# Optimization experiments

Hardware: AMD Instinct MI355X
Metric: run time of the kernel (lower is better)

Reference implementation:

```python
import jax, jax.numpy as jnp
import numpy as np

B, T, C = 2, 2048, 1024
H = 16
D = C // H          # 64
HID = C // 4        # meta_net bottleneck = 256
FF = 4 * C          # 4096


def setup_inputs() -> dict:
    key = jax.random.key(0)
    ks = jax.random.split(key, 11)
    s = lambda fan_in: 1.0 / np.sqrt(fan_in)
    inp = {
        "x": jax.random.normal(ks[0], (B, T, C), jnp.float32),
        # torch nn.Linear weights are [out, in]
        "Wq": jax.random.uniform(ks[1], (C, C), jnp.float32, -s(C), s(C)),
        "Wk": jax.random.uniform(ks[2], (C, C), jnp.float32, -s(C), s(C)),
        "Wv": jax.random.uniform(ks[3], (C, C), jnp.float32, -s(C), s(C)),
        "Wm1": jax.random.uniform(ks[4], (HID, C), jnp.float32, -s(C), s(C)),
        "bm1": jax.random.uniform(ks[5], (HID,), jnp.float32, -s(C), s(C)),
        "Wm2": jax.random.uniform(ks[6], (H, HID), jnp.float32, -s(HID), s(HID)),
        "bm2": jax.random.uniform(ks[7], (H,), jnp.float32, -s(HID), s(HID)),
        "Wproj": jax.random.uniform(ks[8], (C, C), jnp.float32, -s(C), s(C)),
        "Wfc": jax.random.uniform(ks[9], (FF, C), jnp.float32, -s(C), s(C)),
        "Wcp": jax.random.uniform(ks[10], (C, FF), jnp.float32, -s(FF), s(FF)),
    }
    return inp


def _rms_norm(x):
    eps = jnp.finfo(x.dtype).eps
    return x * jax.lax.rsqrt(jnp.mean(jnp.square(x), axis=-1, keepdims=True) + eps)


def reference(x, Wq, Wk, Wv, Wm1, bm1, Wm2, bm2, Wproj, Wfc, Wcp):
    b, t, c = x.shape
    h = Wm2.shape[0]
    d = c // h
    q = (x @ Wq.T).reshape(b, t, h, d)
    k = (x @ Wk.T).reshape(b, t, h, d)
    v = (x @ Wv.T).reshape(b, t, h, d)
    surprise = jax.nn.sigmoid(jnp.maximum(x @ Wm1.T + bm1, 0.0) @ Wm2.T + bm2)  # [b,t,h]
    decay = 1.0 - surprise

    # time-major for scan: [t, b, h, ...]
    qT = jnp.transpose(q, (1, 0, 2, 3))
    kT = jnp.transpose(k, (1, 0, 2, 3))
    vT = jnp.transpose(v, (1, 0, 2, 3))
    dT = jnp.transpose(decay, (1, 0, 2))     # [t,b,h]
    gT = jnp.transpose(surprise, (1, 0, 2))  # [t,b,h]

    def step(state, inp):
        qt, kt, vt, dt, gt = inp
        # state: [b,h,d,d]; decay-gated rank-1 update
        state = state * dt[..., None, None] + gt[..., None, None] * (kt[..., :, None] * vt[..., None, :])
        yt = jnp.einsum('bhd,bhde->bhe', qt, state)
        return state, yt

    state0 = jnp.zeros((b, h, d, d), x.dtype)
    _, ys = jax.lax.scan(step, state0, (qT, kT, vT, dT, gT))  # ys: [t,b,h,d]
    y = jnp.transpose(ys, (1, 0, 2, 3)).reshape(b, t, c)
    y = y @ Wproj.T
    yn = _rms_norm(y)
    mlp = jnp.square(jnp.maximum(yn @ Wfc.T, 0.0)) @ Wcp.T
    return y + mlp
```

## Files before the change

kernel.cpp:

```cpp
#include <hip/hip_runtime.h>
#include <math.h>

#define BB   2
#define TT   2048
#define CC   1024
#define HH   16
#define DD   64
#define HID  256
#define FFD  4096
#define NTOK (BB*TT)
#define CT   64
#define NC   (TT/CT)
#define NBH  (BB*HH)
#define NCHK (NBH*NC)
#define MB   (1048576ULL)

typedef unsigned short u16;
typedef unsigned int   u32;
typedef __attribute__((ext_vector_type(8))) short frag8;
typedef __attribute__((ext_vector_type(4))) float f32x4;

__device__ __forceinline__ float bf2f(u16 h){
    union { u32 u; float f; } c; c.u = ((u32)h) << 16; return c.f;
}
__device__ __forceinline__ u16 f2bf(float f){
    union { float f; u32 u; } c; c.f = f;
    u32 u = c.u;
    u += 0x7FFFu + ((u >> 16) & 1u);
    return (u16)(u >> 16);
}
__device__ __forceinline__ bool is_f32(const u32* flags, int idx) {
    if (idx == -2) return true;
    if (idx < 0)  return false;
    return flags[idx] != 0;
}

__device__ __forceinline__ void gload16(const void* g, void* l) {
    __builtin_amdgcn_global_load_lds(
        (const __attribute__((address_space(1))) u32*)g,
        (__attribute__((address_space(3))) u32*)l, 16, 0, 0);
}

struct InPtrs { const void* p[11]; int n[11]; };

__global__ __launch_bounds__(64)
void sniff_kernel(InPtrs ip, u32* __restrict__ flags)
{
    int lane = threadIdx.x;
    u32 f0 = 0;
    for (int i = 0; i < 11; i++) {
        const u16* p = (const u16*)ip.p[i];
        int cap = ip.n[i] < 256 ? ip.n[i] : 256;
        bool ok = true;
        for (int j = lane; j < cap; j += 64) {
            u16 u = p[j];
            u32 e = (u >> 7) & 0xFFu;
            bool good = (u == 0u) || (u == 0x8000u) || (e >= 64u && e < 192u);
            ok = ok && good;
        }
        unsigned long long ball = __ballot(ok);
        u32 fl = (ball == ~0ull) ? 0u : 1u;
        if (ip.n[i] < 64) fl = f0;
        if (i == 0) f0 = fl;
        if (lane == 0) flags[i] = fl;
    }
}

struct ConvArgs {
    const void* src[6];
    u16* dst[6];
    int flag[6];
    int bstart[7];
    int nseg;
};

__global__ __launch_bounds__(256)
void conv_kernel(ConvArgs a, const u32* __restrict__ flags)
{
    int b = blockIdx.x;
    int s = 0;
    #pragma unroll
    for (int i = 1; i < 6; i++) if (i < a.nseg && b >= a.bstart[i]) s = i;
    size_t off = ((size_t)(b - a.bstart[s])) * 2048 + (size_t)threadIdx.x * 8;
    u16* d = a.dst[s] + off;
    if (flags[a.flag[s]] != 0) {
        const float* sp = (const float*)a.src[s] + off;
        float4 x0 = *(const float4*)sp;
        float4 x1 = *(const float4*)(sp + 4);
        u16 buf[8];
        buf[0]=f2bf(x0.x); buf[1]=f2bf(x0.y); buf[2]=f2bf(x0.z); buf[3]=f2bf(x0.w);
        buf[4]=f2bf(x1.x); buf[5]=f2bf(x1.y); buf[6]=f2bf(x1.z); buf[7]=f2bf(x1.w);
        *(uint4*)d = *(uint4*)buf;
    } else {
        *(uint4*)d = *(const uint4*)((const u16*)a.src[s] + off);
    }
}

__device__ __forceinline__ void xcd_map(int i, int NB, int gx, int& bm, int& bn)
{
    int per = NB >> 3;
    int iq  = (i & 7) * per + (i >> 3);
    bm = iq / gx;
    bn = iq % gx;
}

template<int MODE, int BM, int BN, int KS>
__global__ __launch_bounds__(256)
void gemm_nt(const u16* __restrict__ A, const u16* __restrict__ B,
             void* Cm, void* Cm2, const void* aux,
             int M, int N, int K, int lda, int ldb,
             const u32* __restrict__ flags, int oi)
{
    constexpr int MFR = BM / 32;
    constexpr int NFR = BN / 32;
    constexpr int BKE = KS * 32;
    const bool of32 = is_f32(flags, oi);
    __shared__ u16 As[2][KS][BM * 32];
    __shared__ u16 Bs[2][KS][BN * 32];
    const int tid = threadIdx.x;
    int bm, bn;
    xcd_map(blockIdx.x, gridDim.x, N / BN, bm, bn);
    const int z = blockIdx.y;
    const size_t koff = (size_t)z * K;

    const int wave = tid >> 6, lane = tid & 63;
    const int lm = lane & 15, quad = lane >> 4;
    const int wm = (wave >> 1) * (BM / 2), wn = (wave & 1) * (BN / 2);

    const int srow = lane >> 2;
    const int scol = (lane & 3) * 8;
    const int arow = (BM == 128) ? (wave*32 + srow) : (wave*16 + srow);
    const int brow = (BN == 128) ? (wave*32 + srow) : (wave*16 + srow);
    const u16* gA = A + (size_t)(bm*BM + arow)*lda + koff + scol;
    const u16* gB = B + (size_t)(bn*BN + brow)*ldb + koff + scol;
    const size_t a16 = (size_t)16 * lda, b16 = (size_t)16 * ldb;

    f32x4 acc[MFR][NFR];
    #pragma unroll
    for (int i = 0; i < MFR; i++)
        #pragma unroll
        for (int j = 0; j < NFR; j++)
            acc[i][j] = (f32x4){0.f, 0.f, 0.f, 0.f};

    auto stage = [&](int buf, int kk) {
        #pragma unroll
        for (int ks = 0; ks < KS; ks++) {
            if constexpr (BM == 128) {
                gload16(gA + kk + ks*32,       &As[buf][ks][wave*1024]);
                gload16(gA + kk + ks*32 + a16, &As[buf][ks][wave*1024 + 512]);
            } else {
                gload16(gA + kk + ks*32, &As[buf][ks][wave*512]);
            }
            if constexpr (BN == 128) {
                gload16(gB + kk + ks*32,       &Bs[buf][ks][wave*1024]);
                gload16(gB + kk + ks*32 + b16, &Bs[buf][ks][wave*1024 + 512]);
            } else {
                gload16(gB + kk + ks*32, &Bs[buf][ks][wave*512]);
            }
        }
    };

    stage(0, 0);
    __syncthreads();
    int cur = 0;
    for (int k0 = 0; k0 < K; k0 += BKE) {
        if (k0 + BKE < K) stage(cur ^ 1, k0 + BKE);
        #pragma unroll
        for (int ks = 0; ks < KS; ks++) {
            frag8 af[MFR], bfr[NFR];
            #pragma unroll
            for (int i = 0; i < MFR; i++)
                af[i]  = *(frag8*)&As[cur][ks][(wm + i*16 + lm)*32 + quad*8];
            #pragma unroll
            for (int j = 0; j < NFR; j++)
                bfr[j] = *(frag8*)&Bs[cur][ks][(wn + j*16 + lm)*32 + quad*8];
            #pragma unroll
            for (int i = 0; i < MFR; i++)
                #pragma unroll
                for (int j = 0; j < NFR; j++)
                    acc[i][j] = __builtin_amdgcn_mfma_f32_16x16x32_bf16(
                        af[i], bfr[j], acc[i][j], 0, 0, 0);
        }
        __syncthreads();
        cur ^= 1;
    }

    float* outF = (float*)(z ? Cm2 : Cm);
    #pragma unroll
    for (int i = 0; i < MFR; i++) {
        #pragma unroll
        for (int j = 0; j < NFR; j++) {
            const int gcol = bn*BN + wn + j*16 + lm;
            #pragma unroll
            for (int r = 0; r < 4; r++) {
                const int grow = bm*BM + wm + i*16 + quad*4 + r;
                size_t off = (size_t)grow * N + gcol;
                float vv = acc[i][j][r];
                if constexpr (MODE == 0) {
                    outF[off] = vv;
                } else if constexpr (MODE == 2) {
                    vv = fmaxf(vv, 0.f);
                    ((u16*)Cm)[off] = f2bf(vv * vv);
                } else {
                    float res = of32 ? ((const float*)aux)[off]
                                     : bf2f(((const u16*)aux)[off]);
                    vv += res;
                    if (of32) ((float*)Cm)[off] = vv;
                    else      ((u16*)Cm)[off]   = f2bf(vv);
                }
            }
        }
    }
}

__global__ __launch_bounds__(256)
void gemm_qkvm(const u16* __restrict__ xb,
               const u16* __restrict__ Wqb, const u16* __restrict__ Wkb,
               const u16* __restrict__ Wvb, const u16* __restrict__ Wm1b,
               const void* __restrict__ bm1,
               u16* __restrict__ q, u16* __restrict__ k, u16* __restrict__ v,
               float* __restrict__ hid, const u32* __restrict__ flags)
{
    __shared__ u16 As[2][128 * 32];
    __shared__ u16 Bs[2][128 * 32];
    const int tid = threadIdx.x;
    int bm, bn;
    xcd_map(blockIdx.x, 832, 26, bm, bn);

    const int bsel = bn >> 3;
    const u16* B = (bsel == 0) ? Wqb : (bsel == 1) ? Wkb
                 : (bsel == 2) ? Wvb : Wm1b;

    const int wave = tid >> 6, lane = tid & 63;
    const int lm = lane & 15, quad = lane >> 4;
    const int wm = (wave >> 1) * 64, wn = (wave & 1) * 64;

    const int srow = lane >> 2;
    const int scol = (lane & 3) * 8;
    const u16* gA = xb + (size_t)(bm*128 + wave*32 + srow)*CC + scol;
    const u16* gB = B + (size_t)((bn & 7)*128 + wave*32 + srow)*CC + scol;
    const size_t s16 = (size_t)16 * CC;

    f32x4 acc[4][4];
    #pragma unroll
    for (int i = 0; i < 4; i++)
        #pragma unroll
        for (int j = 0; j < 4; j++)
            acc[i][j] = (f32x4){0.f, 0.f, 0.f, 0.f};

    auto stage = [&](int buf, int kk) {
        gload16(gA + kk,       &As[buf][wave*1024]);
        gload16(gA + kk + s16, &As[buf][wave*1024 + 512]);
        gload16(gB + kk,       &Bs[buf][wave*1024]);
        gload16(gB + kk + s16, &Bs[buf][wave*1024 + 512]);
    };

    stage(0, 0);
    __syncthreads();
    int cur = 0;
    for (int k0 = 0; k0 < CC; k0 += 32) {
        if (k0 + 32 < CC) stage(cur ^ 1, k0 + 32);
        frag8 af[4], bfr[4];
        #pragma unroll
        for (int i = 0; i < 4; i++) {
            af[i]  = *(frag8*)&As[cur][(wm + i*16 + lm)*32 + quad*8];
            bfr[i] = *(frag8*)&Bs[cur][(wn + i*16 + lm)*32 + quad*8];
        }
        #pragma unroll
        for (int i = 0; i < 4; i++)
            #pragma unroll
            for (int j = 0; j < 4; j++)
                acc[i][j] = __builtin_amdgcn_mfma_f32_16x16x32_bf16(
                    af[i], bfr[j], acc[i][j], 0, 0, 0);
        __syncthreads();
        cur ^= 1;
    }

    if (bsel < 3) {
        u16* outp = (bsel == 0) ? q : (bsel == 1) ? k : v;
        #pragma unroll
        for (int i = 0; i < 4; i++) {
            #pragma unroll
            for (int j = 0; j < 4; j++) {
                const int gcol = (bn & 7)*128 + wn + j*16 + lm;
                #pragma unroll
                for (int r = 0; r < 4; r++) {
                    const int grow = bm*128 + wm + i*16 + quad*4 + r;
                    outp[(size_t)grow * CC + gcol] = f2bf(acc[i][j][r]);
                }
            }
        }
    } else {
        const bool biasf = is_f32(flags, 5);
        #pragma unroll
        for (int i = 0; i < 4; i++) {
            #pragma unroll
            for (int j = 0; j < 4; j++) {
                const int gcol = (bn & 7)*128 + wn + j*16 + lm;
                float bia = biasf ? ((const float*)bm1)[gcol]
                                  : bf2f(((const u16*)bm1)[gcol]);
                #pragma unroll
                for (int r = 0; r < 4; r++) {
                    const int grow = bm*128 + wm + i*16 + quad*4 + r;
                    hid[(size_t)grow * HID + gcol] = fmaxf(acc[i][j][r] + bia, 0.f);
                }
            }
        }
    }
}

__global__ __launch_bounds__(256)
void meta2_kernel(const float* __restrict__ hid, const void* __restrict__ Wm2,
                  const void* __restrict__ bm2, float* __restrict__ g,
                  float* __restrict__ dec, const u32* __restrict__ flags)
{
    const bool wf = is_f32(flags, 6);
    const bool bf = is_f32(flags, 7);
    __shared__ float hs[16][257];
    __shared__ float wsm[16][257];
    int tid  = threadIdx.x;
    int tok0 = blockIdx.x * 16;
    for (int i = tid; i < 16*256; i += 256) {
        wsm[i >> 8][i & 255] = wf ? ((const float*)Wm2)[i] : bf2f(((const u16*)Wm2)[i]);
        hs [i >> 8][i & 255] = hid[(size_t)tok0*256 + i];
    }
    __syncthreads();
    int tok = tid >> 4, hh = tid & 15;
    float s = 0.f;
    #pragma unroll 8
    for (int kk = 0; kk < 256; kk++) s = fmaf(hs[tok][kk], wsm[hh][kk], s);
    s += bf ? ((const float*)bm2)[hh] : bf2f(((const u16*)bm2)[hh]);
    float sg = 1.f / (1.f + expf(-s));
    int idx = (tok0 + tok) * HH + hh;
    g[idx]   = sg;
    dec[idx] = 1.f - sg;
}

__device__ __forceinline__ void cum_prefix(const float* dd, float* cum, int tid)
{
    if (tid < 64) {
        float lw = logf(fmaxf(dd[tid], 1e-30f));
        #pragma unroll
        for (int off = 1; off < 64; off <<= 1) {
            float nv = __shfl_up(lw, off, 64);
            if (tid >= off) lw += nv;
        }
        cum[tid] = lw;
    }
    __syncthreads();
}

__global__ __launch_bounds__(256)
void scan_pass1(const u16* __restrict__ kbuf, const u16* __restrict__ vbuf,
                const float* __restrict__ g, const float* __restrict__ dec,
                float* __restrict__ Mb, float* __restrict__ Pb)
{
    __shared__ float ks[64*64];
    __shared__ float vs[64*64];
    __shared__ float dd[64], gg[64], cum[64], sw[64];
    int tid = threadIdx.x;
    int bhc = blockIdx.x;
    int c = bhc & 31, h = (bhc >> 5) & 15, b = bhc >> 9;
    int t0 = c * CT;
    size_t rowbase = ((size_t)(b*TT + t0))*CC + h*DD;

    for (int i = tid; i < 4096; i += 256) {
        int s = i >> 6, d = i & 63;
        ks[i] = bf2f(kbuf[rowbase + (size_t)s*CC + d]);
        vs[i] = bf2f(vbuf[rowbase + (size_t)s*CC + d]);
    }
    if (tid < 64) {
        int gidx = (b*TT + t0 + tid)*HH + h;
        dd[tid] = dec[gidx];
        gg[tid] = g[gidx];
    }
    __syncthreads();
    cum_prefix(dd, cum, tid);
    float ctot = cum[63];
    if (tid < 64) sw[tid] = gg[tid] * expf(ctot - cum[tid]);
    __syncthreads();

    int d0 = (tid >> 4) * 4, e0 = (tid & 15) * 4;
    float m[4][4] = {};
    for (int s = 0; s < 64; s++) {
        float w = sw[s];
        float4 kv = *(const float4*)&ks[s*64 + d0];
        float4 vv = *(const float4*)&vs[s*64 + e0];
        float a0 = w*kv.x, a1 = w*kv.y, a2 = w*kv.z, a3 = w*kv.w;
        m[0][0]=fmaf(a0,vv.x,m[0][0]); m[0][1]=fmaf(a0,vv.y,m[0][1]); m[0][2]=fmaf(a0,vv.z,m[0][2]); m[0][3]=fmaf(a0,vv.w,m[0][3]);
        m[1][0]=fmaf(a1,vv.x,m[1][0]); m[1][1]=fmaf(a1,vv.y,m[1][1]); m[1][2]=fmaf(a1,vv.z,m[1][2]); m[1][3]=fmaf(a1,vv.w,m[1][3]);
        m[2][0]=fmaf(a2,vv.x,m[2][0]); m[2][1]=fmaf(a2,vv.y,m[2][1]); m[2][2]=fmaf(a2,vv.z,m[2][2]); m[2][3]=fmaf(a2,vv.w,m[2][3]);
        m[3][0]=fmaf(a3,vv.x,m[3][0]); m[3][1]=fmaf(a3,vv.y,m[3][1]); m[3][2]=fmaf(a3,vv.z,m[3][2]); m[3][3]=fmaf(a3,vv.w,m[3][3]);
    }
    size_t base = (size_t)bhc * 4096;
    #pragma unroll
    for (int i = 0; i < 4; i++) {
        float4 o = make_float4(m[i][0], m[i][1], m[i][2], m[i][3]);
        *(float4*)&Mb[base + (size_t)(d0 + i)*64 + e0] = o;
    }
    if (tid == 0) Pb[bhc] = expf(ctot);
}

__global__ __launch_bounds__(256)
void scan_pass2(float* __restrict__ MS, const float* __restrict__ Pb)
{
    int bh = blockIdx.x >> 4, grp = blockIdx.x & 15, tid = threadIdx.x;
    int eo = grp*256 + tid;
    float st = 0.f;
    for (int c = 0; c < NC; c++) {
        size_t e = ((size_t)bh*NC + c) * 4096 + eo;
        float p = Pb[bh*NC + c];
        float m = MS[e];
        MS[e] = st;
        st = fmaf(p, st, m);
    }
}

__global__ __launch_bounds__(256)
void scan_pass3(const u16* __restrict__ qbuf, const u16* __restrict__ kbuf,
                const u16* __restrict__ vbuf, const float* __restrict__ g,
                const float* __restrict__ dec, const float* __restrict__ Sb,
                u16* __restrict__ y)
{
    __shared__ float qs[64*64];
    __shared__ float kt[64*68];
    __shared__ float vs[64*64];
    __shared__ u16   Aws[4096];
    __shared__ float dd[64], gg[64], cum[64];
    int tid = threadIdx.x;
    int bhc = blockIdx.x;
    int c = bhc & 31, h = (bhc >> 5) & 15, b = bhc >> 9;
    int t0 = c * CT;
    size_t rowbase = ((size_t)(b*TT + t0))*CC + h*DD;

    for (int i = tid; i < 4096; i += 256) {
        int s = i >> 6, d = i & 63;
        size_t gi = rowbase + (size_t)s*CC + d;
        qs[i]        = bf2f(qbuf[gi]);
        kt[d*68 + s] = bf2f(kbuf[gi]);
        vs[i]        = bf2f(vbuf[gi]);
    }
    if (tid < 64) {
        int gidx = (b*TT + t0 + tid)*HH + h;
        dd[tid] = dec[gidx];
        gg[tid] = g[gidx];
    }
    __syncthreads();
    cum_prefix(dd, cum, tid);

    const int tt0 = (tid >> 4) * 4, ss0 = (tid & 15) * 4;
    float a1[4][4] = {};
    for (int d = 0; d < 64; d++) {
        float4 kv = *(const float4*)&kt[d*68 + ss0];
        #pragma unroll
        for (int i = 0; i < 4; i++) {
            float qv = qs[(tt0 + i)*64 + d];
            a1[i][0] = fmaf(qv, kv.x, a1[i][0]);
            a1[i][1] = fmaf(qv, kv.y, a1[i][1]);
            a1[i][2] = fmaf(qv, kv.z, a1[i][2]);
            a1[i][3] = fmaf(qv, kv.w, a1[i][3]);
        }
    }
    #pragma unroll
    for (int i = 0; i < 4; i++) {
        int t = tt0 + i;
        float ct = cum[t];
        #pragma unroll
        for (int j = 0; j < 4; j++) {
            int s = ss0 + j;
            float w = (s <= t) ? gg[s] * expf(ct - cum[s]) : 0.f;
            Aws[t*64 + s] = f2bf(w * a1[i][j]);
        }
    }
    __syncthreads();
    float* Ss = kt;
    size_t sbase = (size_t)bhc * 4096;
    for (int i = tid; i < 4096; i += 256) Ss[i] = Sb[sbase + i];
    __syncthreads();

    const int e0 = ss0;
    float o1[4][4] = {}, o2[4][4] = {};
    for (int s = 0; s < 64; s++) {
        float4 vv = *(const float4*)&vs[s*64 + e0];
        #pragma unroll
        for (int i = 0; i < 4; i++) {
            float av = bf2f(Aws[(tt0 + i)*64 + s]);
            o1[i][0] = fmaf(av, vv.x, o1[i][0]);
            o1[i][1] = fmaf(av, vv.y, o1[i][1]);
            o1[i][2] = fmaf(av, vv.z, o1[i][2]);
            o1[i][3] = fmaf(av, vv.w, o1[i][3]);
        }
    }
    for (int d = 0; d < 64; d++) {
        float4 sv = *(const float4*)&Ss[d*64 + e0];
        #pragma unroll
        for (int i = 0; i < 4; i++) {
            float qv = qs[(tt0 + i)*64 + d];
            o2[i][0] = fmaf(qv, sv.x, o2[i][0]);
            o2[i][1] = fmaf(qv, sv.y, o2[i][1]);
            o2[i][2] = fmaf(qv, sv.z, o2[i][2]);
            o2[i][3] = fmaf(qv, sv.w, o2[i][3]);
        }
    }
    #pragma unroll
    for (int i = 0; i < 4; i++) {
        float cd = expf(cum[tt0 + i]);
        size_t obase = rowbase + (size_t)(tt0 + i)*CC + e0;
        #pragma unroll
        for (int j = 0; j < 4; j++)
            y[obase + j] = f2bf(fmaf(cd, o2[i][j], o1[i][j]));
    }
}

__global__ __launch_bounds__(256)
void rmsnorm_kernel(const float* __restrict__ p0, const float* __restrict__ p1,
                    void* __restrict__ yres, u16* __restrict__ yn,
                    const u32* __restrict__ flags)
{
    const bool of32 = flags[0] != 0;
    __shared__ float red[4];
    __shared__ float sscale;
    int row = blockIdx.x, tid = threadIdx.x;
    size_t base = (size_t)row*CC + tid*4;
    float4 a = *(const float4*)&p0[base];
    float4 b = *(const float4*)&p1[base];
    float v0 = a.x + b.x, v1 = a.y + b.y, v2 = a.z + b.z, v3 = a.w + b.w;
    if (of32) {
        *(float4*)((float*)yres + base) = make_float4(v0, v1, v2, v3);
    } else {
        u16* yr = (u16*)yres + base;
        yr[0] = f2bf(v0); yr[1] = f2bf(v1); yr[2] = f2bf(v2); yr[3] = f2bf(v3);
    }
    float p = v0*v0 + v1*v1 + v2*v2 + v3*v3;
    #pragma unroll
    for (int off = 32; off > 0; off >>= 1) p += __shfl_down(p, off, 64);
    if ((tid & 63) == 0) red[tid >> 6] = p;
    __syncthreads();
    if (tid == 0) {
        float tot = red[0] + red[1] + red[2] + red[3];
        sscale = rsqrtf(tot * (1.0f/1024.0f) + 1.1920928955078125e-07f);
    }
    __syncthreads();
    float sc = sscale;
    yn[base + 0] = f2bf(v0 * sc);
    yn[base + 1] = f2bf(v1 * sc);
    yn[base + 2] = f2bf(v2 * sc);
    yn[base + 3] = f2bf(v3 * sc);
}

extern "C" void kernel_launch(void* const* d_in, const int* in_sizes, int n_in,
                              void* d_out, int out_size, void* d_ws, size_t ws_size,
                              hipStream_t stream)
{
    char* ws = (char*)d_ws;
    u16*   xb     = (u16*)  (ws + 32*MB);
    u16*   Wqb    = (u16*)  (ws + 40*MB);
    u16*   Wkb    = (u16*)  (ws + 42*MB);
    u16*   Wvb    = (u16*)  (ws + 44*MB);
    u16*   Wm1b   = (u16*)  (ws + 46*MB);
    u16*   Wprojb = (u16*)  (ws + 8*MB);
    u16*   q      = (u16*)  (ws + 0*MB);
    u16*   k      = (u16*)  (ws + 16*MB);
    u16*   v      = (u16*)  (ws + 24*MB);
    float* hid    = (float*)(ws + 10*MB);
    float* g      = (float*)(ws + 14*MB);
    float* dec    = (float*)(ws + 14*MB + 262144);
    float* Pb     = (float*)(ws + 14*MB + 524288);
    float* MS     = (float*)(ws + 32*MB);
    u16*   yat    = q;
    float* p0     = (float*)(ws + 16*MB);
    float* p1     = (float*)(ws + 32*MB);
    u16*   yn     = (u16*)  (ws + 0*MB);
    u16*   Wfcb   = (u16*)  (ws + 8*MB);
    u16*   h1     = (u16*)  (ws + 16*MB);
    u16*   Wcpb   = (u16*)  (ws + 0*MB);
    u32*   flags  = (u32*)  (ws + 48*MB);

    InPtrs ip;
    for (int i = 0; i < 11; i++) { ip.p[i] = d_in[i]; ip.n[i] = in_sizes[i]; }
    sniff_kernel<<<1, 64, 0, stream>>>(ip, flags);

    ConvArgs c1{};
    c1.src[0] = d_in[0]; c1.dst[0] = xb;     c1.flag[0] = 0;
    c1.src[1] = d_in[1]; c1.dst[1] = Wqb;    c1.flag[1] = 1;
    c1.src[2] = d_in[2]; c1.dst[2] = Wkb;    c1.flag[2] = 2;
    c1.src[3] = d_in[3]; c1.dst[3] = Wvb;    c1.flag[3] = 3;
    c1.src[4] = d_in[4]; c1.dst[4] = Wm1b;   c1.flag[4] = 4;
    c1.src[5] = d_in[8]; c1.dst[5] = Wprojb; c1.flag[5] = 8;
    {
        int nb[6] = {2048, 512, 512, 512, 128, 512};
        int cum = 0;
        for (int i = 0; i < 6; i++) { c1.bstart[i] = cum; cum += nb[i]; }
        c1.bstart[6] = cum;
        c1.nseg = 6;
        conv_kernel<<<cum, 256, 0, stream>>>(c1, flags);
    }

    gemm_qkvm<<<832, 256, 0, stream>>>(xb, Wqb, Wkb, Wvb, Wm1b, d_in[5],
                                       q, k, v, hid, flags);
    meta2_kernel<<<NTOK/16, 256, 0, stream>>>(hid, d_in[6], d_in[7], g, dec, flags);
    scan_pass1<<<NCHK, 256, 0, stream>>>(k, v, g, dec, MS, Pb);
    scan_pass2<<<NBH*16, 256, 0, stream>>>(MS, Pb);
    scan_pass3<<<NCHK, 256, 0, stream>>>(q, k, v, g, dec, MS, yat);
    gemm_nt<0,128,128,1><<<dim3(256, 2), 256, 0, stream>>>(yat, Wprojb, p0, p1,
        nullptr, NTOK, CC, 512, CC, CC, flags, -2);
    ConvArgs c2{};
    c2.src[0] = d_in[9]; c2.dst[0] = Wfcb; c2.flag[0] = 9;
    c2.bstart[0] = 0; for (int i = 1; i < 7; i++) c2.bstart[i] = 2048;
    c2.nseg = 1;
    conv_kernel<<<2048, 256, 0, stream>>>(c2, flags);
    rmsnorm_kernel<<<NTOK, 256, 0, stream>>>(p0, p1, d_out, yn, flags);
    gemm_nt<2,128,128,1><<<dim3(1024, 1), 256, 0, stream>>>(yn, Wfcb, h1, nullptr,
        nullptr, NTOK, FFD, CC, CC, CC, flags, -1);
    ConvArgs c3{};
    c3.src[0] = d_in[10]; c3.dst[0] = Wcpb; c3.flag[0] = 10;
    c3.bstart[0] = 0; for (int i = 1; i < 7; i++) c3.bstart[i] = 2048;
    c3.nseg = 1;
    conv_kernel<<<2048, 256, 0, stream>>>(c3, flags);
    gemm_nt<3,64,64,2><<<dim3(1024, 1), 256, 0, stream>>>(h1, Wcpb, d_out, nullptr,
        d_out, NTOK, CC, FFD, FFD, FFD, flags, 0);
}
```

Baseline: 397.5 us.

## Use bf16 MFMA for intra-chunk QK^T and AV in scan_pass3

Rewrites the chunk output kernel so the Q·K^T and A·V products use 16x16x32 bf16 MFMA instructions. Q, K and V stay in bf16 in padded shared memory instead of being widened to fp32. The carried state is loaded transposed into shared memory up front, which removes one barrier. The state product Q·S stays in fp32 FMAs but now follows the MFMA output layout. The aim is to cut scalar FMA work and shared-memory footprint in the scan stage, at the cost of a strided transposed V store and a reorganised output layout.

Result: faster. 388.2 us (-2.4%).

```diff
diff --git a/kernel.cpp b/kernel.cpp
--- a/kernel.cpp
+++ b/kernel.cpp
@@ -422,93 +422,123 @@
                 const float* __restrict__ dec, const float* __restrict__ Sb,
                 u16* __restrict__ y)
 {
-    __shared__ float qs[64*64];
-    __shared__ float kt[64*68];
-    __shared__ float vs[64*64];
-    __shared__ u16   Aws[4096];
+    __shared__ u16 qs16[64*72];
+    __shared__ u16 ks16[64*72];
+    __shared__ u16 vt16[64*72];
+    __shared__ u16 aws16[64*72];
+    __shared__ float Ss_t[64*68];
     __shared__ float dd[64], gg[64], cum[64];
     int tid = threadIdx.x;
     int bhc = blockIdx.x;
     int c = bhc & 31, h = (bhc >> 5) & 15, b = bhc >> 9;
     int t0 = c * CT;
     size_t rowbase = ((size_t)(b*TT + t0))*CC + h*DD;
-
-    for (int i = tid; i < 4096; i += 256) {
-        int s = i >> 6, d = i & 63;
-        size_t gi = rowbase + (size_t)s*CC + d;
-        qs[i]        = bf2f(qbuf[gi]);
-        kt[d*68 + s] = bf2f(kbuf[gi]);
-        vs[i]        = bf2f(vbuf[gi]);
-    }
-    if (tid < 64) {
-        int gidx = (b*TT + t0 + tid)*HH + h;
-        dd[tid] = dec[gidx];
-        gg[tid] = g[gidx];
+    size_t sbase = (size_t)bhc * 4096;
+
+    {
+        int sr = tid >> 2, d0 = (tid & 3) * 16;
+        size_t gq = rowbase + (size_t)sr*CC + d0;
+        *(uint4*)&qs16[sr*72 + d0]     = *(const uint4*)&qbuf[gq];
+        *(uint4*)&qs16[sr*72 + d0 + 8] = *(const uint4*)&qbuf[gq + 8];
+        *(uint4*)&ks16[sr*72 + d0]     = *(const uint4*)&kbuf[gq];
+        *(uint4*)&ks16[sr*72 + d0 + 8] = *(const uint4*)&kbuf[gq + 8];
+        #pragma unroll 4
+        for (int i = tid; i < 4096; i += 256) {
+            int ss = i >> 6, e = i & 63;
+            vt16[e*72 + ss] = vbuf[rowbase + (size_t)ss*CC + e];
+        }
+        int dr = tid >> 2, e0 = (tid & 3) * 16;
+        #pragma unroll
+        for (int m = 0; m < 4; m++) {
+            float4 sv4 = *(const float4*)&Sb[sbase + (size_t)dr*64 + e0 + m*4];
+            Ss_t[(e0 + m*4 + 0)*68 + dr] = sv4.x;
+            Ss_t[(e0 + m*4 + 1)*68 + dr] = sv4.y;
+            Ss_t[(e0 + m*4 + 2)*68 + dr] = sv4.z;
+            Ss_t[(e0 + m*4 + 3)*68 + dr] = sv4.w;
+        }
+        if (tid < 64) {
+            int gidx = (b*TT + t0 + tid)*HH + h;
+            dd[tid] = dec[gidx];
+            gg[tid] = g[gidx];
+        }
     }
     __syncthreads();
     cum_prefix(dd, cum, tid);
 
-    const int tt0 = (tid >> 4) * 4, ss0 = (tid & 15) * 4;
-    float a1[4][4] = {};
-    for (int d = 0; d < 64; d++) {
-        float4 kv = *(const float4*)&kt[d*68 + ss0];
-        #pragma unroll
-        for (int i = 0; i < 4; i++) {
-            float qv = qs[(tt0 + i)*64 + d];
-            a1[i][0] = fmaf(qv, kv.x, a1[i][0]);
-            a1[i][1] = fmaf(qv, kv.y, a1[i][1]);
-            a1[i][2] = fmaf(qv, kv.z, a1[i][2]);
-            a1[i][3] = fmaf(qv, kv.w, a1[i][3]);
-        }
-    }
-    #pragma unroll
-    for (int i = 0; i < 4; i++) {
-        int t = tt0 + i;
-        float ct = cum[t];
+    const int w = tid >> 6, lane = tid & 63;
+    const int lm = lane & 15, quad = lane >> 4;
+
+    f32x4 a1f[4];
+    #pragma unroll
+    for (int j = 0; j < 4; j++) a1f[j] = (f32x4){0.f,0.f,0.f,0.f};
+    #pragma unroll
+    for (int kk = 0; kk < 2; kk++) {
+        frag8 aq = *(frag8*)&qs16[(w*16 + lm)*72 + kk*32 + quad*8];
         #pragma unroll
         for (int j = 0; j < 4; j++) {
-            int s = ss0 + j;
-            float w = (s <= t) ? gg[s] * expf(ct - cum[s]) : 0.f;
-            Aws[t*64 + s] = f2bf(w * a1[i][j]);
-        }
-    }
-    __syncthreads();
-    float* Ss = kt;
-    size_t sbase = (size_t)bhc * 4096;
-    for (int i = tid; i < 4096; i += 256) Ss[i] = Sb[sbase + i];
-    __syncthreads();
-
-    const int e0 = ss0;
-    float o1[4][4] = {}, o2[4][4] = {};
-    for (int s = 0; s < 64; s++) {
-        float4 vv = *(const float4*)&vs[s*64 + e0];
-        #pragma unroll
-        for (int i = 0; i < 4; i++) {
-            float av = bf2f(Aws[(tt0 + i)*64 + s]);
-            o1[i][0] = fmaf(av, vv.x, o1[i][0]);
-            o1[i][1] = fmaf(av, vv.y, o1[i][1]);
-            o1[i][2] = fmaf(av, vv.z, o1[i][2]);
-            o1[i][3] = fmaf(av, vv.w, o1[i][3]);
-        }
-    }
-    for (int d = 0; d < 64; d++) {
-        float4 sv = *(const float4*)&Ss[d*64 + e0];
-        #pragma unroll
-        for (int i = 0; i < 4; i++) {
-            float qv = qs[(tt0 + i)*64 + d];
-            o2[i][0] = fmaf(qv, sv.x, o2[i][0]);
-            o2[i][1] = fmaf(qv, sv.y, o2[i][1]);
-            o2[i][2] = fmaf(qv, sv.z, o2[i][2]);
-            o2[i][3] = fmaf(qv, sv.w, o2[i][3]);
-        }
-    }
-    #pragma unroll
-    for (int i = 0; i < 4; i++) {
-        float cd = expf(cum[tt0 + i]);
-        size_t obase = rowbase + (size_t)(tt0 + i)*CC + e0;
+            frag8 bk = *(frag8*)&ks16[(j*16 + lm)*72 + kk*32 + quad*8];
+            a1f[j] = __builtin_amdgcn_mfma_f32_16x16x32_bf16(aq, bk, a1f[j], 0, 0, 0);
+        }
+    }
+
+    #pragma unroll
+    for (int j = 0; j < 4; j++) {
+        #pragma unroll
+        for (int r = 0; r < 4; r++) {
+            int t = w*16 + quad*4 + r, s = j*16 + lm;
+            float wgt = (s <= t) ? gg[s] * expf(cum[t] - cum[s]) : 0.f;
+            aws16[t*72 + s] = f2bf(wgt * a1f[j][r]);
+        }
+    }
+    __syncthreads();
+
+    f32x4 of[4];
+    #pragma unroll
+    for (int j = 0; j < 4; j++) of[j] = (f32x4){0.f,0.f,0.f,0.f};
+    #pragma unroll
+    for (int kk = 0; kk < 2; kk++) {
+        frag8 aA = *(frag8*)&aws16[(w*16 + lm)*72 + kk*32 + quad*8];
+        #pragma unroll
+        for (int j = 0; j < 4; j++) {
+            frag8 bV = *(frag8*)&vt16[(j*16 + lm)*72 + kk*32 + quad*8];
+            of[j] = __builtin_amdgcn_mfma_f32_16x16x32_bf16(aA, bV, of[j], 0, 0, 0);
+        }
+    }
+
+    float o2v[4][4] = {};
+    for (int d8 = 0; d8 < 8; d8++) {
+        frag8 qr[4];
+        #pragma unroll
+        for (int r = 0; r < 4; r++)
+            qr[r] = *(frag8*)&qs16[(w*16 + quad*4 + r)*72 + d8*8];
+        float qv[4][8];
+        #pragma unroll
+        for (int r = 0; r < 4; r++)
+            #pragma unroll
+            for (int d2 = 0; d2 < 8; d2++)
+                qv[r][d2] = bf2f((u16)qr[r][d2]);
+        #pragma unroll
+        for (int j = 0; j < 4; j++) {
+            int e = j*16 + lm;
+            float4 s0 = *(float4*)&Ss_t[e*68 + d8*8];
+            float4 s1 = *(float4*)&Ss_t[e*68 + d8*8 + 4];
+            float sv[8] = {s0.x, s0.y, s0.z, s0.w, s1.x, s1.y, s1.z, s1.w};
+            #pragma unroll
+            for (int d2 = 0; d2 < 8; d2++)
+                #pragma unroll
+                for (int r = 0; r < 4; r++)
+                    o2v[j][r] = fmaf(qv[r][d2], sv[d2], o2v[j][r]);
+        }
+    }
+
+    #pragma unroll
+    for (int r = 0; r < 4; r++) {
+        int t = w*16 + quad*4 + r;
+        float cd = expf(cum[t]);
+        size_t obase = rowbase + (size_t)t*CC;
         #pragma unroll
         for (int j = 0; j < 4; j++)
-            y[obase + j] = f2bf(fmaf(cd, o2[i][j], o1[i][j]));
+            y[obase + j*16 + lm] = f2bf(fmaf(cd, o2v[j][r], of[j][r]));
     }
 }
 
```
